# Performance work log

Hardware: AMD Instinct MI355X
Metric: run time of the kernel (lower is better)

The kernel has to match this reference:

```python
import jax, jax.numpy as jnp
import numpy as np

N_TAYLOR = 4

def taylor_exp_poly(x, n_terms):
    # sum_{p=0}^{n_terms-1} x^p / p!  via Horner: 1 + x*(1 + x/2*(1 + x/3*(...)))
    acc = jnp.ones_like(x)
    for p in range(n_terms - 1, 0, -1):
        acc = 1.0 + (x / p) * acc
    return acc

def setup_inputs() -> dict:
    key = jax.random.key(0)
    kq, kk, kv = jax.random.split(key, 3)
    B, H, T, d_key, d_val = 4, 8, 2048, 32, 64
    Q = jax.random.normal(kq, (B, H, T, d_key), dtype=jnp.float32)
    K = jax.random.normal(kk, (B, H, T, d_key), dtype=jnp.float32)
    V = jax.random.normal(kv, (B, H, T, d_val), dtype=jnp.float32)
    return {"Q": Q, "K": K, "V": V}

def reference(Q, K, V):
    # Symmetry-aware Taylor-approximated attention (Heinsen & Kozachkov).
    # The tightly-packed degree-p feature maps phi_p satisfy
    #   phi_p(q) . phi_p(k) == (q.k / sqrt(d_key))^p / p!
    # so summing S/Z over all n_taylor terms equals attention with kernel
    #   w(q,k) = sum_{p<n_taylor} (q.k/sqrt(d_key))^p / p!   (truncated exp),
    # causally masked and normalized by the row-sum Z.
    d_key = Q.shape[-1]
    scale = 1.0 / jnp.sqrt(jnp.asarray(d_key, dtype=Q.dtype))
    scores = jnp.einsum('bhqd,bhkd->bhqk', Q, K) * scale  # [B,H,T,T]
    A = taylor_exp_poly(scores, N_TAYLOR)
    T = Q.shape[-2]
    causal = jnp.tril(jnp.ones((T, T), dtype=bool))  # [T,T]
    A = jnp.where(causal, A, jnp.zeros((), dtype=A.dtype))
    Z = jnp.sum(A, axis=-1, keepdims=True)           # [B,H,T,1]
    S = jnp.einsum('bhqk,bhkd->bhqd', A, V)          # [B,H,T,d_val]
    return S / Z
```

## Files before the change

### kernel.cpp

```cpp
#include <hip/hip_runtime.h>
#include <hip/hip_bf16.h>


typedef __attribute__((ext_vector_type(8))) short bf16x8;
typedef __attribute__((ext_vector_type(16))) float f32x16;
typedef unsigned int u32;
typedef unsigned short u16;

namespace {

constexpr int T_SEQ = 2048;
constexpr int DK    = 32;
constexpr int DV    = 64;
constexpr int NBH   = 32;

constexpr float C1 = 0.17677669529663687f;
constexpr float C2 = 0.015625f;
constexpr float C3 = 9.2071195e-4f;

constexpr size_t KHI_OFF  = 0;
constexpr size_t KLO_OFF  = (size_t)NBH * T_SEQ * DK * 2;
constexpr size_t VTHI_OFF = KLO_OFF * 2;
constexpr size_t WS_NEED  = VTHI_OFF + (size_t)NBH * DV * T_SEQ * 2;

__device__ __forceinline__ u32 pack_hi2(float f0, float f1) {
  return (__float_as_uint(f0) >> 16) | (__float_as_uint(f1) & 0xffff0000u);
}
__device__ __forceinline__ float trunc_bf(float f) {
  return __uint_as_float(__float_as_uint(f) & 0xffff0000u);
}
__device__ __forceinline__ u16 bfhi(float f) { return (u16)(__float_as_uint(f) >> 16); }

__device__ __forceinline__ u32 pack_rn2(float f0, float f1) {
  union { __hip_bfloat16 h; u16 u; } a, b;
  a.h = __hip_bfloat16(f0);
  b.h = __hip_bfloat16(f1);
  return (u32)a.u | ((u32)b.u << 16);
}

__device__ __forceinline__ void permswap(u32& a, u32& b) {
  asm volatile("v_permlane32_swap_b32 %0, %1" : "+v"(a), "+v"(b));
}


__global__ void pack_kv(const float* __restrict__ Kg, const float* __restrict__ Vg,
                        u16* __restrict__ Khi, u16* __restrict__ Klo,
                        u16* __restrict__ Vthi) {
  __shared__ float tile[DV][33];
  const int bid = blockIdx.x;
  const int t   = threadIdx.x;
  if (bid < 2048) {
    size_t i = ((size_t)bid * 256 + t) * 4;
    float4 f = *(const float4*)(Kg + i);
    ushort4 h, l;
    h.x = bfhi(f.x); h.y = bfhi(f.y); h.z = bfhi(f.z); h.w = bfhi(f.w);
    l.x = bfhi(f.x - trunc_bf(f.x)); l.y = bfhi(f.y - trunc_bf(f.y));
    l.z = bfhi(f.z - trunc_bf(f.z)); l.w = bfhi(f.w - trunc_bf(f.w));
    *(ushort4*)(Khi + i) = h;
    *(ushort4*)(Klo + i) = l;
  } else {
    const int vb = bid - 2048;
    const int bh = vb >> 6;
    const int k0 = (vb & 63) * 32;
    {
      const int kl = t >> 3, c0 = (t & 7) * 8;
      const float* src = Vg + ((size_t)bh * T_SEQ + k0 + kl) * DV + c0;
      float4 a = *(const float4*)src;
      float4 b = *(const float4*)(src + 4);
      tile[c0 + 0][kl] = a.x; tile[c0 + 1][kl] = a.y;
      tile[c0 + 2][kl] = a.z; tile[c0 + 3][kl] = a.w;
      tile[c0 + 4][kl] = b.x; tile[c0 + 5][kl] = b.y;
      tile[c0 + 6][kl] = b.z; tile[c0 + 7][kl] = b.w;
    }
    __syncthreads();
    {
      const int cl = t >> 2, k8 = (t & 3) * 8;
      u32 h[4];
#pragma unroll
      for (int j = 0; j < 4; ++j)
        h[j] = pack_rn2(tile[cl][k8 + 2 * j], tile[cl][k8 + 2 * j + 1]);
      size_t off = ((size_t)(bh * DV + cl)) * T_SEQ + k0 + k8;
      *(uint4*)(Vthi + off) = make_uint4(h[0], h[1], h[2], h[3]);
    }
  }
}


__global__ __launch_bounds__(128, 4)
void taylor_attn_v5(const float* __restrict__ Qg, const u16* __restrict__ Khi,
                    const u16* __restrict__ Klo, const u16* __restrict__ Vthi,
                    float* __restrict__ Outg) {
  __shared__ __align__(16) float Sp[32 * 64];
  __shared__ float Zp[64];

  const int tid = threadIdx.x;
  const int l   = tid & 63;
  const int w   = tid >> 6;
  const int cq  = l & 31;
  const int hi  = l >> 5;

  const int bid = blockIdx.x;
  const int xcd = bid & 7;
  const int u   = bid >> 3;
  const int j   = u >> 5;
  const int c   = u & 31;
  const int bh  = xcd * 4 + (j & 3);
  const int s   = (j >= 4) ? (63 - 2 * c) : (2 * c);
  const int q0  = s * 32;

  const int nsteps = s + 1;
  const int half   = (nsteps + 1) >> 1;
  const int kt0    = w ? half : 0;
  const int kt1    = w ? nsteps : half;

  bf16x8 qfh[2], qfl[2];
#pragma unroll
  for (int t = 0; t < 2; ++t) {
    const float* qp = Qg + ((size_t)bh * T_SEQ + q0 + cq) * DK + t * 16 + hi * 8;
    float4 a = *(const float4*)qp;
    float4 b = *(const float4*)(qp + 4);
    union { bf16x8 v; u32 u[4]; } H, L;
    H.u[0] = pack_hi2(a.x, a.y); H.u[1] = pack_hi2(a.z, a.w);
    H.u[2] = pack_hi2(b.x, b.y); H.u[3] = pack_hi2(b.z, b.w);
    L.u[0] = pack_hi2(a.x - trunc_bf(a.x), a.y - trunc_bf(a.y));
    L.u[1] = pack_hi2(a.z - trunc_bf(a.z), a.w - trunc_bf(a.w));
    L.u[2] = pack_hi2(b.x - trunc_bf(b.x), b.y - trunc_bf(b.y));
    L.u[3] = pack_hi2(b.z - trunc_bf(b.z), b.w - trunc_bf(b.w));
    qfh[t] = H.v; qfl[t] = L.v;
  }

  f32x16 acc[2];
#pragma unroll
  for (int ct = 0; ct < 2; ++ct)
#pragma unroll
    for (int r = 0; r < 16; ++r) acc[ct][r] = 0.f;
  float zacc = 0.f;

  const u16* kbh_hi = Khi + (size_t)bh * T_SEQ * DK;
  const u16* kbh_lo = Klo + (size_t)bh * T_SEQ * DK;
  const u16* vbh_hi = Vthi + (size_t)bh * DV * T_SEQ;

  for (int kt = kt0; kt < kt1; ++kt) {
    const int k0 = kt * 32;

    bf16x8 kfh[2], kfl[2];
#pragma unroll
    for (int t = 0; t < 2; ++t) {
      size_t off = (size_t)(k0 + cq) * DK + t * 16 + hi * 8;
      kfh[t] = *(const bf16x8*)(kbh_hi + off);
      kfl[t] = *(const bf16x8*)(kbh_lo + off);
    }

    f32x16 d0, d1;
#pragma unroll
    for (int r = 0; r < 16; ++r) { d0[r] = 0.f; d1[r] = 0.f; }
    d0 = __builtin_amdgcn_mfma_f32_32x32x16_bf16(kfh[0], qfh[0], d0, 0, 0, 0);
    d1 = __builtin_amdgcn_mfma_f32_32x32x16_bf16(kfh[1], qfh[1], d1, 0, 0, 0);
    d0 = __builtin_amdgcn_mfma_f32_32x32x16_bf16(kfh[0], qfl[0], d0, 0, 0, 0);
    d1 = __builtin_amdgcn_mfma_f32_32x32x16_bf16(kfh[1], qfl[1], d1, 0, 0, 0);
    d0 = __builtin_amdgcn_mfma_f32_32x32x16_bf16(kfl[0], qfh[0], d0, 0, 0, 0);
    d1 = __builtin_amdgcn_mfma_f32_32x32x16_bf16(kfl[1], qfh[1], d1, 0, 0, 0);

    float wv[16];
    const bool diag = (kt == s);
#pragma unroll
    for (int r = 0; r < 16; ++r) {
      float sc = d0[r] + d1[r];
      float t_ = __builtin_fmaf(sc, C3, C2);
      t_       = __builtin_fmaf(sc, t_, C1);
      float wr = __builtin_fmaf(sc, t_, 1.0f);
      if (diag) {
        const int krel = (r & 3) + 8 * (r >> 2) + 4 * hi;
        wr = (krel <= cq) ? wr : 0.f;
      }
      zacc += wr;
      wv[r] = wr;
    }

    union { bf16x8 v; u32 u[4]; } WH[2];
#pragma unroll
    for (int t = 0; t < 2; ++t) {
      const int b = t * 8;
      u32 p0 = pack_rn2(wv[b + 0], wv[b + 1]);
      u32 p1 = pack_rn2(wv[b + 2], wv[b + 3]);
      u32 p2 = pack_rn2(wv[b + 4], wv[b + 5]);
      u32 p3 = pack_rn2(wv[b + 6], wv[b + 7]);
      permswap(p0, p2); permswap(p1, p3);
      WH[t].u[0] = p0; WH[t].u[1] = p1; WH[t].u[2] = p2; WH[t].u[3] = p3;
    }

#pragma unroll
    for (int ct = 0; ct < 2; ++ct) {
#pragma unroll
      for (int t = 0; t < 2; ++t) {
        size_t voff = (size_t)(ct * 32 + cq) * T_SEQ + k0 + t * 16 + hi * 8;
        bf16x8 vh = *(const bf16x8*)(vbh_hi + voff);
        acc[ct] = __builtin_amdgcn_mfma_f32_32x32x16_bf16(WH[t].v, vh, acc[ct], 0, 0, 0);
      }
    }
  }

  {
    float zt = zacc + __shfl_xor(zacc, 32);
    if (hi == 0) Zp[w * 32 + cq] = zt;
  }
  if (w == 1) {
#pragma unroll
    for (int ct = 0; ct < 2; ++ct)
#pragma unroll
      for (int r = 0; r < 16; ++r) {
        const int qr = (r & 3) + 8 * (r >> 2) + 4 * hi;
        Sp[qr * 64 + ct * 32 + cq] = acc[ct][r];
      }
  }
  __syncthreads();

  if (w == 0) {
    float zinv[16];
#pragma unroll
    for (int r = 0; r < 16; ++r) {
      const int qr = (r & 3) + 8 * (r >> 2) + 4 * hi;
      zinv[r] = 1.0f / (Zp[qr] + Zp[32 + qr]);
    }
#pragma unroll
    for (int ct = 0; ct < 2; ++ct)
#pragma unroll
      for (int r = 0; r < 16; ++r) {
        const int qr = (r & 3) + 8 * (r >> 2) + 4 * hi;
        float o = (acc[ct][r] + Sp[qr * 64 + ct * 32 + cq]) * zinv[r];
        Outg[((size_t)bh * T_SEQ + q0 + qr) * DV + ct * 32 + cq] = o;
      }
  }
}


constexpr int QT_FB = 64;
constexpr int KT_FB = 32;
constexpr int LDSW  = 40;
constexpr float SCALE = 0.17677669529663687f;

__global__ __launch_bounds__(256, 4)
void taylor_attn_fb(const float* __restrict__ Qg, const float* __restrict__ Kg,
                    const float* __restrict__ Vg, float* __restrict__ Outg) {
  __shared__ __align__(16) unsigned short Qhi[QT_FB * LDSW], Qlo[QT_FB * LDSW];
  __shared__ __align__(16) unsigned short Khi_[KT_FB * LDSW], Klo_[KT_FB * LDSW];
  __shared__ __align__(16) unsigned short Vthi_[DV * LDSW], Vtlo_[DV * LDSW];
  __shared__ __align__(16) unsigned Wp[4][16 * 32];

  const int tid  = threadIdx.x;
  const int lane = tid & 63;
  const int wid  = tid >> 6;
  const int m    = lane & 15;
  const int g    = lane >> 4;

  const int bid = blockIdx.x;
  const int v   = bid >> 3;
  const int bh  = (bid & 7) * 4 + (v >> 5);
  const int qt  = 31 - (v & 31);
  const int q0  = qt * QT_FB;

  const float* Qbase = Qg + ((size_t)bh * T_SEQ + q0) * DK;
  const float* Kbase = Kg + (size_t)bh * T_SEQ * DK;
  const float* Vbase = Vg + (size_t)bh * T_SEQ * DV;

#pragma unroll
  for (int p = 0; p < 2; ++p) {
    int e = tid + p * 256, row = e >> 3, c4 = (e & 7) * 4;
    float4 f = *(const float4*)(Qbase + row * DK + c4);
    uint2 h, l;
    h.x = pack_hi2(f.x, f.y); h.y = pack_hi2(f.z, f.w);
    l.x = pack_hi2(f.x - trunc_bf(f.x), f.y - trunc_bf(f.y));
    l.y = pack_hi2(f.z - trunc_bf(f.z), f.w - trunc_bf(f.w));
    *(uint2*)&Qhi[row * LDSW + c4] = h;
    *(uint2*)&Qlo[row * LDSW + c4] = l;
  }
  __syncthreads();

  const int wq = wid * 16;
  const bf16x8 qhi = *(const bf16x8*)&Qhi[(wq + m) * LDSW + g * 8];
  const bf16x8 qlo = *(const bf16x8*)&Qlo[(wq + m) * LDSW + g * 8];

  typedef __attribute__((ext_vector_type(4))) float f32x4;
  f32x4 acc[4];
#pragma unroll
  for (int ct = 0; ct < 4; ++ct) acc[ct] = f32x4{0.f, 0.f, 0.f, 0.f};
  float zacc[4] = {0.f, 0.f, 0.f, 0.f};

  const int q_lane0 = q0 + wq + g * 4;
  const int q_wave_max = q0 + wq + 15;

  const int nkt = (q0 + QT_FB) / KT_FB;
  for (int kt = 0; kt < nkt; ++kt) {
    const int k0 = kt * KT_FB;
    __syncthreads();
    {
      int row = tid >> 3, c4 = (tid & 7) * 4;
      float4 f = *(const float4*)(Kbase + (size_t)(k0 + row) * DK + c4);
      uint2 h, l;
      h.x = pack_hi2(f.x, f.y); h.y = pack_hi2(f.z, f.w);
      l.x = pack_hi2(f.x - trunc_bf(f.x), f.y - trunc_bf(f.y));
      l.y = pack_hi2(f.z - trunc_bf(f.z), f.w - trunc_bf(f.w));
      *(uint2*)&Khi_[row * LDSW + c4] = h;
      *(uint2*)&Klo_[row * LDSW + c4] = l;
    }
    {
      int kk = (tid & 15) * 2, c4 = (tid >> 4) * 4;
      const float* vp = Vbase + (size_t)(k0 + kk) * DV + c4;
      float4 a = *(const float4*)vp;
      float4 b = *(const float4*)(vp + DV);
      float af[4] = {a.x, a.y, a.z, a.w};
      float bf_[4] = {b.x, b.y, b.z, b.w};
#pragma unroll
      for (int jj = 0; jj < 4; ++jj) {
        *(unsigned*)&Vthi_[(c4 + jj) * LDSW + kk] = pack_hi2(af[jj], bf_[jj]);
        *(unsigned*)&Vtlo_[(c4 + jj) * LDSW + kk] =
            pack_hi2(af[jj] - trunc_bf(af[jj]), bf_[jj] - trunc_bf(bf_[jj]));
      }
    }
    __syncthreads();

    if (k0 > q_wave_max) continue;

#pragma unroll
    for (int k16 = 0; k16 < 2; ++k16) {
      const int kcol0 = k16 * 16;
      bf16x8 khi = *(const bf16x8*)&Khi_[(kcol0 + m) * LDSW + g * 8];
      bf16x8 klo = *(const bf16x8*)&Klo_[(kcol0 + m) * LDSW + g * 8];
      f32x4 sc = {0.f, 0.f, 0.f, 0.f};
      sc = __builtin_amdgcn_mfma_f32_16x16x32_bf16(qhi, khi, sc, 0, 0, 0);
      sc = __builtin_amdgcn_mfma_f32_16x16x32_bf16(qhi, klo, sc, 0, 0, 0);
      sc = __builtin_amdgcn_mfma_f32_16x16x32_bf16(qlo, khi, sc, 0, 0, 0);
      const int k_abs = k0 + kcol0 + m;
      const int kcol  = kcol0 + m;
#pragma unroll
      for (int r = 0; r < 4; ++r) {
        float x  = sc[r] * SCALE;
        float a3 = __builtin_fmaf(x, 0.3333333333333333f, 1.0f);
        float a2 = __builtin_fmaf(x * 0.5f, a3, 1.0f);
        float wv = __builtin_fmaf(x, a2, 1.0f);
        wv = (k_abs <= q_lane0 + r) ? wv : 0.0f;
        zacc[r] += wv;
        float wl = wv - trunc_bf(wv);
        unsigned packed = (__float_as_uint(wv) >> 16) |
                          (__float_as_uint(wl) & 0xffff0000u);
        const int q = g * 4 + r;
        Wp[wid][q * 32 + (((kcol >> 2) ^ (q & 7)) << 2) + (kcol & 3)] = packed;
      }
    }

    uint4 pa = *(const uint4*)&Wp[wid][m * 32 + (((2 * g) ^ (m & 7)) << 2)];
    uint4 pb = *(const uint4*)&Wp[wid][m * 32 + (((2 * g + 1) ^ (m & 7)) << 2)];
    union { bf16x8 v; unsigned u[4]; } WH, WL;
    WH.u[0] = (pa.x & 0xffffu) | (pa.y << 16);
    WH.u[1] = (pa.z & 0xffffu) | (pa.w << 16);
    WH.u[2] = (pb.x & 0xffffu) | (pb.y << 16);
    WH.u[3] = (pb.z & 0xffffu) | (pb.w << 16);
    WL.u[0] = (pa.x >> 16) | (pa.y & 0xffff0000u);
    WL.u[1] = (pa.z >> 16) | (pa.w & 0xffff0000u);
    WL.u[2] = (pb.x >> 16) | (pb.y & 0xffff0000u);
    WL.u[3] = (pb.z >> 16) | (pb.w & 0xffff0000u);

#pragma unroll
    for (int ct = 0; ct < 4; ++ct) {
      bf16x8 vhi = *(const bf16x8*)&Vthi_[(ct * 16 + m) * LDSW + g * 8];
      bf16x8 vlo = *(const bf16x8*)&Vtlo_[(ct * 16 + m) * LDSW + g * 8];
      acc[ct] = __builtin_amdgcn_mfma_f32_16x16x32_bf16(WH.v, vhi, acc[ct], 0, 0, 0);
      acc[ct] = __builtin_amdgcn_mfma_f32_16x16x32_bf16(WH.v, vlo, acc[ct], 0, 0, 0);
      acc[ct] = __builtin_amdgcn_mfma_f32_16x16x32_bf16(WL.v, vhi, acc[ct], 0, 0, 0);
    }
  }

  float invz[4];
#pragma unroll
  for (int r = 0; r < 4; ++r) {
    float z = zacc[r];
    z += __shfl_xor(z, 1); z += __shfl_xor(z, 2);
    z += __shfl_xor(z, 4); z += __shfl_xor(z, 8);
    invz[r] = 1.0f / z;
  }

  float* ob = Outg + ((size_t)bh * T_SEQ + (q0 + wq)) * DV;
#pragma unroll
  for (int ct = 0; ct < 4; ++ct)
#pragma unroll
    for (int r = 0; r < 4; ++r)
      ob[(g * 4 + r) * DV + ct * 16 + m] = acc[ct][r] * invz[r];
}

}

extern "C" void kernel_launch(void* const* d_in, const int* in_sizes, int n_in,
                              void* d_out, int out_size, void* d_ws, size_t ws_size,
                              hipStream_t stream) {
  const float* Q = (const float*)d_in[0];
  const float* K = (const float*)d_in[1];
  const float* V = (const float*)d_in[2];
  float* Out = (float*)d_out;

  if (ws_size >= WS_NEED && d_ws != nullptr) {
    u16* khi  = (u16*)((char*)d_ws + KHI_OFF);
    u16* klo  = (u16*)((char*)d_ws + KLO_OFF);
    u16* vthi = (u16*)((char*)d_ws + VTHI_OFF);

    hipLaunchKernelGGL(pack_kv, dim3(4096), dim3(256), 0, stream,
                       K, V, khi, klo, vthi);
    hipLaunchKernelGGL(taylor_attn_v5, dim3(2048), dim3(128), 0, stream,
                       Q, khi, klo, vthi, Out);
  } else {
    hipLaunchKernelGGL(taylor_attn_fb, dim3(1024), dim3(256), 0, stream,
                       Q, K, V, Out);
  }
}
```

Measured before the change: 68.19 us.

## Pair complementary causal tiles per block and split key loop across four waves

The attention kernel now runs 256-thread blocks that each process two query tiles, s and 63-s, in sequence, so every block does the same total causal work. The key tiles are strided across four waves instead of split in halves across two. The partial S and Z values from all four waves are reduced through a larger LDS buffer, and the output is written with vectorized float4 stores. V fragments are also loaded ahead of the score MFMAs to hide latency. The cost is 32KB of LDS per block, which may limit occupancy, plus extra barriers between the two phases.

```diff
diff --git a/kernel.cpp b/kernel.cpp
--- a/kernel.cpp
+++ b/kernel.cpp
@@ -3,6 +3,7 @@
 
 
 typedef __attribute__((ext_vector_type(8))) short bf16x8;
+typedef __attribute__((ext_vector_type(4))) float f32x4;
 typedef __attribute__((ext_vector_type(16))) float f32x16;
 typedef unsigned int u32;
 typedef unsigned short u16;
@@ -86,12 +87,12 @@
 }
 
 
-__global__ __launch_bounds__(128, 4)
-void taylor_attn_v5(const float* __restrict__ Qg, const u16* __restrict__ Khi,
+__global__ __launch_bounds__(256, 4)
+void taylor_attn_v6(const float* __restrict__ Qg, const u16* __restrict__ Khi,
                     const u16* __restrict__ Klo, const u16* __restrict__ Vthi,
                     float* __restrict__ Outg) {
-  __shared__ __align__(16) float Sp[32 * 64];
-  __shared__ float Zp[64];
+  __shared__ __align__(16) float Sp[4 * 2048];
+  __shared__ float Zp[4 * 32];
 
   const int tid = threadIdx.x;
   const int l   = tid & 63;
@@ -101,135 +102,135 @@
 
   const int bid = blockIdx.x;
   const int xcd = bid & 7;
-  const int u   = bid >> 3;
-  const int j   = u >> 5;
-  const int c   = u & 31;
-  const int bh  = xcd * 4 + (j & 3);
-  const int s   = (j >= 4) ? (63 - 2 * c) : (2 * c);
-  const int q0  = s * 32;
-
-  const int nsteps = s + 1;
-  const int half   = (nsteps + 1) >> 1;
-  const int kt0    = w ? half : 0;
-  const int kt1    = w ? nsteps : half;
-
-  bf16x8 qfh[2], qfl[2];
-#pragma unroll
-  for (int t = 0; t < 2; ++t) {
-    const float* qp = Qg + ((size_t)bh * T_SEQ + q0 + cq) * DK + t * 16 + hi * 8;
-    float4 a = *(const float4*)qp;
-    float4 b = *(const float4*)(qp + 4);
-    union { bf16x8 v; u32 u[4]; } H, L;
-    H.u[0] = pack_hi2(a.x, a.y); H.u[1] = pack_hi2(a.z, a.w);
-    H.u[2] = pack_hi2(b.x, b.y); H.u[3] = pack_hi2(b.z, b.w);
-    L.u[0] = pack_hi2(a.x - trunc_bf(a.x), a.y - trunc_bf(a.y));
-    L.u[1] = pack_hi2(a.z - trunc_bf(a.z), a.w - trunc_bf(a.w));
-    L.u[2] = pack_hi2(b.x - trunc_bf(b.x), b.y - trunc_bf(b.y));
-    L.u[3] = pack_hi2(b.z - trunc_bf(b.z), b.w - trunc_bf(b.w));
-    qfh[t] = H.v; qfl[t] = L.v;
-  }
-
-  f32x16 acc[2];
-#pragma unroll
-  for (int ct = 0; ct < 2; ++ct)
-#pragma unroll
-    for (int r = 0; r < 16; ++r) acc[ct][r] = 0.f;
-  float zacc = 0.f;
+  const int r_  = bid >> 3;
+  const int bh  = xcd * 4 + (r_ & 3);
+  const int p   = r_ >> 2;
 
   const u16* kbh_hi = Khi + (size_t)bh * T_SEQ * DK;
   const u16* kbh_lo = Klo + (size_t)bh * T_SEQ * DK;
   const u16* vbh_hi = Vthi + (size_t)bh * DV * T_SEQ;
-
-  for (int kt = kt0; kt < kt1; ++kt) {
-    const int k0 = kt * 32;
-
-    bf16x8 kfh[2], kfl[2];
+  const float* qb   = Qg + (size_t)bh * T_SEQ * DK;
+
+#pragma unroll 1
+  for (int ph = 0; ph < 2; ++ph) {
+    const int s  = ph ? (63 - p) : p;
+    const int q0 = s * 32;
+
+    if (ph) __syncthreads();
+
+    bf16x8 qfh[2], qfl[2];
 #pragma unroll
     for (int t = 0; t < 2; ++t) {
-      size_t off = (size_t)(k0 + cq) * DK + t * 16 + hi * 8;
-      kfh[t] = *(const bf16x8*)(kbh_hi + off);
-      kfl[t] = *(const bf16x8*)(kbh_lo + off);
-    }
-
-    f32x16 d0, d1;
-#pragma unroll
-    for (int r = 0; r < 16; ++r) { d0[r] = 0.f; d1[r] = 0.f; }
-    d0 = __builtin_amdgcn_mfma_f32_32x32x16_bf16(kfh[0], qfh[0], d0, 0, 0, 0);
-    d1 = __builtin_amdgcn_mfma_f32_32x32x16_bf16(kfh[1], qfh[1], d1, 0, 0, 0);
-    d0 = __builtin_amdgcn_mfma_f32_32x32x16_bf16(kfh[0], qfl[0], d0, 0, 0, 0);
-    d1 = __builtin_amdgcn_mfma_f32_32x32x16_bf16(kfh[1], qfl[1], d1, 0, 0, 0);
-    d0 = __builtin_amdgcn_mfma_f32_32x32x16_bf16(kfl[0], qfh[0], d0, 0, 0, 0);
-    d1 = __builtin_amdgcn_mfma_f32_32x32x16_bf16(kfl[1], qfh[1], d1, 0, 0, 0);
-
-    float wv[16];
-    const bool diag = (kt == s);
-#pragma unroll
-    for (int r = 0; r < 16; ++r) {
-      float sc = d0[r] + d1[r];
-      float t_ = __builtin_fmaf(sc, C3, C2);
-      t_       = __builtin_fmaf(sc, t_, C1);
-      float wr = __builtin_fmaf(sc, t_, 1.0f);
-      if (diag) {
-        const int krel = (r & 3) + 8 * (r >> 2) + 4 * hi;
-        wr = (krel <= cq) ? wr : 0.f;
-      }
-      zacc += wr;
-      wv[r] = wr;
-    }
-
-    union { bf16x8 v; u32 u[4]; } WH[2];
-#pragma unroll
-    for (int t = 0; t < 2; ++t) {
-      const int b = t * 8;
-      u32 p0 = pack_rn2(wv[b + 0], wv[b + 1]);
-      u32 p1 = pack_rn2(wv[b + 2], wv[b + 3]);
-      u32 p2 = pack_rn2(wv[b + 4], wv[b + 5]);
-      u32 p3 = pack_rn2(wv[b + 6], wv[b + 7]);
-      permswap(p0, p2); permswap(p1, p3);
-      WH[t].u[0] = p0; WH[t].u[1] = p1; WH[t].u[2] = p2; WH[t].u[3] = p3;
-    }
-
-#pragma unroll
-    for (int ct = 0; ct < 2; ++ct) {
+      const float* qp = qb + (size_t)(q0 + cq) * DK + t * 16 + hi * 8;
+      float4 a = *(const float4*)qp;
+      float4 b = *(const float4*)(qp + 4);
+      union { bf16x8 v; u32 u[4]; } H, L;
+      H.u[0] = pack_hi2(a.x, a.y); H.u[1] = pack_hi2(a.z, a.w);
+      H.u[2] = pack_hi2(b.x, b.y); H.u[3] = pack_hi2(b.z, b.w);
+      L.u[0] = pack_hi2(a.x - trunc_bf(a.x), a.y - trunc_bf(a.y));
+      L.u[1] = pack_hi2(a.z - trunc_bf(a.z), a.w - trunc_bf(a.w));
+      L.u[2] = pack_hi2(b.x - trunc_bf(b.x), b.y - trunc_bf(b.y));
+      L.u[3] = pack_hi2(b.z - trunc_bf(b.z), b.w - trunc_bf(b.w));
+      qfh[t] = H.v; qfl[t] = L.v;
+    }
+
+    f32x16 acc[2];
+#pragma unroll
+    for (int ct = 0; ct < 2; ++ct)
+#pragma unroll
+      for (int r = 0; r < 16; ++r) acc[ct][r] = 0.f;
+    float zacc = 0.f;
+
+    for (int kt = w; kt <= s; kt += 4) {
+      const int k0 = kt * 32;
+
+      bf16x8 kfh[2], kfl[2];
 #pragma unroll
       for (int t = 0; t < 2; ++t) {
-        size_t voff = (size_t)(ct * 32 + cq) * T_SEQ + k0 + t * 16 + hi * 8;
-        bf16x8 vh = *(const bf16x8*)(vbh_hi + voff);
-        acc[ct] = __builtin_amdgcn_mfma_f32_32x32x16_bf16(WH[t].v, vh, acc[ct], 0, 0, 0);
-      }
-    }
-  }
-
-  {
-    float zt = zacc + __shfl_xor(zacc, 32);
-    if (hi == 0) Zp[w * 32 + cq] = zt;
-  }
-  if (w == 1) {
+        size_t off = (size_t)(k0 + cq) * DK + t * 16 + hi * 8;
+        kfh[t] = *(const bf16x8*)(kbh_hi + off);
+        kfl[t] = *(const bf16x8*)(kbh_lo + off);
+      }
+      bf16x8 vfr[4];
+#pragma unroll
+      for (int ct = 0; ct < 2; ++ct)
+#pragma unroll
+        for (int t = 0; t < 2; ++t)
+          vfr[ct * 2 + t] = *(const bf16x8*)(
+              vbh_hi + (size_t)(ct * 32 + cq) * T_SEQ + k0 + t * 16 + hi * 8);
+
+      f32x16 d0, d1;
+#pragma unroll
+      for (int r = 0; r < 16; ++r) { d0[r] = 0.f; d1[r] = 0.f; }
+      d0 = __builtin_amdgcn_mfma_f32_32x32x16_bf16(kfh[0], qfh[0], d0, 0, 0, 0);
+      d1 = __builtin_amdgcn_mfma_f32_32x32x16_bf16(kfh[1], qfh[1], d1, 0, 0, 0);
+      d0 = __builtin_amdgcn_mfma_f32_32x32x16_bf16(kfh[0], qfl[0], d0, 0, 0, 0);
+      d1 = __builtin_amdgcn_mfma_f32_32x32x16_bf16(kfh[1], qfl[1], d1, 0, 0, 0);
+      d0 = __builtin_amdgcn_mfma_f32_32x32x16_bf16(kfl[0], qfh[0], d0, 0, 0, 0);
+      d1 = __builtin_amdgcn_mfma_f32_32x32x16_bf16(kfl[1], qfh[1], d1, 0, 0, 0);
+
+      float wv[16];
+      const bool diag = (kt == s);
+#pragma unroll
+      for (int r = 0; r < 16; ++r) {
+        float sc = d0[r] + d1[r];
+        float t_ = __builtin_fmaf(sc, C3, C2);
+        t_       = __builtin_fmaf(sc, t_, C1);
+        float wr = __builtin_fmaf(sc, t_, 1.0f);
+        if (diag) {
+          const int krel = (r & 3) + 8 * (r >> 2) + 4 * hi;
+          wr = (krel <= cq) ? wr : 0.f;
+        }
+        zacc += wr;
+        wv[r] = wr;
+      }
+
+      union { bf16x8 v; u32 u[4]; } WH[2];
+#pragma unroll
+      for (int t = 0; t < 2; ++t) {
+        const int b = t * 8;
+        u32 p0 = pack_rn2(wv[b + 0], wv[b + 1]);
+        u32 p1 = pack_rn2(wv[b + 2], wv[b + 3]);
+        u32 p2 = pack_rn2(wv[b + 4], wv[b + 5]);
+        u32 p3 = pack_rn2(wv[b + 6], wv[b + 7]);
+        permswap(p0, p2); permswap(p1, p3);
+        WH[t].u[0] = p0; WH[t].u[1] = p1; WH[t].u[2] = p2; WH[t].u[3] = p3;
+      }
+
+#pragma unroll
+      for (int ct = 0; ct < 2; ++ct)
+#pragma unroll
+        for (int t = 0; t < 2; ++t)
+          acc[ct] = __builtin_amdgcn_mfma_f32_32x32x16_bf16(WH[t].v, vfr[ct * 2 + t],
+                                                            acc[ct], 0, 0, 0);
+    }
+
+    {
+      float zt = zacc + __shfl_xor(zacc, 32);
+      if (hi == 0) Zp[w * 32 + cq] = zt;
+    }
 #pragma unroll
     for (int ct = 0; ct < 2; ++ct)
 #pragma unroll
       for (int r = 0; r < 16; ++r) {
         const int qr = (r & 3) + 8 * (r >> 2) + 4 * hi;
-        Sp[qr * 64 + ct * 32 + cq] = acc[ct][r];
-      }
-  }
-  __syncthreads();
-
-  if (w == 0) {
-    float zinv[16];
-#pragma unroll
-    for (int r = 0; r < 16; ++r) {
-      const int qr = (r & 3) + 8 * (r >> 2) + 4 * hi;
-      zinv[r] = 1.0f / (Zp[qr] + Zp[32 + qr]);
-    }
-#pragma unroll
-    for (int ct = 0; ct < 2; ++ct)
-#pragma unroll
-      for (int r = 0; r < 16; ++r) {
-        const int qr = (r & 3) + 8 * (r >> 2) + 4 * hi;
-        float o = (acc[ct][r] + Sp[qr * 64 + ct * 32 + cq]) * zinv[r];
-        Outg[((size_t)bh * T_SEQ + q0 + qr) * DV + ct * 32 + cq] = o;
-      }
+        Sp[w * 2048 + qr * 64 + ct * 32 + cq] = acc[ct][r];
+      }
+    __syncthreads();
+
+    const f32x4* S4 = (const f32x4*)Sp;
+#pragma unroll
+    for (int i = 0; i < 2; ++i) {
+      const int e4  = tid + i * 256;
+      const int row = e4 >> 4;
+      f32x4 ssum = S4[e4] + S4[512 + e4] + S4[1024 + e4] + S4[1536 + e4];
+      float z = Zp[row] + Zp[32 + row] + Zp[64 + row] + Zp[96 + row];
+      float inv = 1.0f / z;
+      float4 o;
+      o.x = ssum[0] * inv; o.y = ssum[1] * inv;
+      o.z = ssum[2] * inv; o.w = ssum[3] * inv;
+      *(float4*)(Outg + ((size_t)bh * T_SEQ + q0 + row) * DV + (e4 & 15) * 4) = o;
+    }
   }
 }
 
@@ -280,7 +281,6 @@
   const bf16x8 qhi = *(const bf16x8*)&Qhi[(wq + m) * LDSW + g * 8];
   const bf16x8 qlo = *(const bf16x8*)&Qlo[(wq + m) * LDSW + g * 8];
 
-  typedef __attribute__((ext_vector_type(4))) float f32x4;
   f32x4 acc[4];
 #pragma unroll
   for (int ct = 0; ct < 4; ++ct) acc[ct] = f32x4{0.f, 0.f, 0.f, 0.f};
@@ -337,11 +337,11 @@
         float x  = sc[r] * SCALE;
         float a3 = __builtin_fmaf(x, 0.3333333333333333f, 1.0f);
         float a2 = __builtin_fmaf(x * 0.5f, a3, 1.0f);
-        float wv = __builtin_fmaf(x, a2, 1.0f);
-        wv = (k_abs <= q_lane0 + r) ? wv : 0.0f;
-        zacc[r] += wv;
-        float wl = wv - trunc_bf(wv);
-        unsigned packed = (__float_as_uint(wv) >> 16) |
+        float wvv = __builtin_fmaf(x, a2, 1.0f);
+        wvv = (k_abs <= q_lane0 + r) ? wvv : 0.0f;
+        zacc[r] += wvv;
+        float wl = wvv - trunc_bf(wvv);
+        unsigned packed = (__float_as_uint(wvv) >> 16) |
                           (__float_as_uint(wl) & 0xffff0000u);
         const int q = g * 4 + r;
         Wp[wid][q * 32 + (((kcol >> 2) ^ (q & 7)) << 2) + (kcol & 3)] = packed;
@@ -404,7 +404,7 @@
 
     hipLaunchKernelGGL(pack_kv, dim3(4096), dim3(256), 0, stream,
                        K, V, khi, klo, vthi);
-    hipLaunchKernelGGL(taylor_attn_v5, dim3(2048), dim3(128), 0, stream,
+    hipLaunchKernelGGL(taylor_attn_v6, dim3(1024), dim3(256), 0, stream,
                        Q, khi, klo, vthi, Out);
   } else {
     hipLaunchKernelGGL(taylor_attn_fb, dim3(1024), dim3(256), 0, stream,
```

Measured after the change: 63.08 us. 1.08x faster.
